# Optimization experiments

Measured on AMD Instinct MI355X. Metric: run time of the kernel, lower is better.

## Reference

```python
import jax, jax.numpy as jnp
import numpy as np

D = 256   # hidden_dim
N = 1024  # total nodes
NP = 384  # paratope nodes
NE = 384  # epitope nodes
NC = 14   # atom channels


def setup_inputs() -> dict:
    key = jax.random.key(0)
    ks = jax.random.split(key, 24)
    s = 1.0 / np.sqrt(D)
    s3 = 1.0 / np.sqrt(3 * D)
    w = lambda k, shape, sc: (jax.random.normal(k, shape, jnp.float32) * sc)
    z = lambda: jnp.zeros((D,), jnp.float32)
    return {
        "H": w(ks[0], (N, D), 1.0),
        "X": w(ks[1], (N, NC, 3), 1.0),
        "paratope_mask": jnp.zeros((N,), bool).at[:NP].set(True),
        "epitope_mask": jnp.zeros((N,), bool).at[NP:NP + NE].set(True),
        "res_w1": w(ks[2], (1, D), 1.0), "res_b1": z(),
        "res_w2": w(ks[3], (D, D), s), "res_b2": z(),
        "atom_w1": w(ks[4], (1, D), 1.0), "atom_b1": z(),
        "atom_w2": w(ks[5], (D, D), s), "atom_b2": z(),
        "sim_weight": jnp.float32(0.5),
        "int_w1": w(ks[6], (3 * D, D), s3), "int_b1": z(),
        "int_w2": w(ks[7], (D, D), s), "int_b2": z(),
        "wl": w(ks[8], (D, D), s),
        "wr": w(ks[9], (D, D), s),
        "wg_w": w(ks[10], (D, D), s), "wg_b": z(),
        "wq_w": w(ks[11], (D, D), s), "wq_b": z(),
        "wk_w": w(ks[12], (D, D), s), "wk_b": z(),
        "wv_w": w(ks[13], (D, D), s), "wv_b": z(),
    }


def _mlp2(x, w1, b1, w2, b2):
    return jax.nn.silu(x @ w1 + b1) @ w2 + b2


def reference(H, X, paratope_mask, epitope_mask,
              res_w1, res_b1, res_w2, res_b2,
              atom_w1, atom_b1, atom_w2, atom_b2,
              sim_weight,
              int_w1, int_b1, int_w2, int_b2,
              wl, wr, wg_w, wg_b, wq_w, wq_b, wk_w, wk_b, wv_w, wv_b):
    p_idx = jnp.nonzero(paratope_mask, size=NP)[0]
    e_idx = jnp.nonzero(epitope_mask, size=NE)[0]
    Hp = H[p_idx]                      # [NP, D]
    He = H[e_idx]                      # [NE, D]
    Xp_ca = X[p_idx, 1]                # [NP, 3] (CA atom)
    Xe_ca = X[e_idx, 1]                # [NE, 3]

    dX = Xp_ca[:, None, :] - Xe_ca[None, :, :]         # [NP, NE, 3]
    S = jnp.sum(dX * dX, axis=-1, keepdims=True)       # [NP, NE, 1]
    # original computes S_residue and S_atom with identical formula
    S_res = _mlp2(S, res_w1, res_b1, res_w2, res_b2)
    S_atom = _mlp2(S, atom_w1, atom_b1, atom_w2, atom_b2)
    wmix = jax.nn.sigmoid(sim_weight)
    S_comb = wmix * S_res + (1.0 - wmix) * S_atom      # [NP, NE, D]

    Hp_e = jnp.broadcast_to(Hp[:, None, :], (NP, NE, D))
    He_e = jnp.broadcast_to(He[None, :, :], (NP, NE, D))
    Z_in = jnp.concatenate([Hp_e, He_e, S_comb], axis=-1)  # [NP, NE, 3D]
    Z = _mlp2(Z_in, int_w1, int_b1, int_w2, int_b2)        # [NP, NE, D]

    I = (Hp @ wl)[:, None, :] * (He @ wr)[None, :, :]      # outer-product interaction
    gate = jax.nn.sigmoid(Z @ wg_w + wg_b)
    f_tri = gate * I

    Q = Z @ wq_w + wq_b
    K = Z @ wk_w + wk_b
    V = Z @ wv_w + wv_b
    scores = jnp.einsum('ped,pfd->pef', Q, K) / (D ** 0.5)  # [NP, NE, NE]
    A = jax.nn.softmax(scores, axis=-1)
    f_att = jnp.einsum('pef,pfd->ped', A, V)

    H_tri = f_tri + f_att                                   # [NP, NE, D]
    return H.at[p_idx].set(H_tri.mean(axis=1))
```

## Files before the change

kernel.cpp:

```cpp
#include <hip/hip_runtime.h>

#define NPAR 384
#define NEPI 384
#define DD   256
#define NTAB 4096
#define SMAX 96.0f
#define SDELTA (SMAX / NTAB)
#define SINVD (NTAB / SMAX)

using bf16x8 = __bf16 __attribute__((ext_vector_type(8)));
using bf16x2 = __bf16 __attribute__((ext_vector_type(2)));
using f32x4  = float __attribute__((ext_vector_type(4)));

#if defined(__has_builtin)
#if __has_builtin(__builtin_amdgcn_cvt_pk_bf16_f32)
#define HAVE_PK_BF16 1
#endif
#endif

__device__ __forceinline__ float sigm(float x) { return 1.0f / (1.0f + __expf(-x)); }
__device__ __forceinline__ float silu(float x) { return x / (1.0f + __expf(-x)); }
__device__ __forceinline__ unsigned short f2bf(float f) {
  unsigned u = __float_as_uint(f);
  u += 0x7fffu + ((u >> 16) & 1u);
  return (unsigned short)(u >> 16);
}
__device__ __forceinline__ float bf2f(unsigned u16) {
  return __uint_as_float(u16 << 16);
}
__device__ __forceinline__ float bf2f_lo(unsigned w) {
  return __uint_as_float(w << 16);
}
__device__ __forceinline__ float bf2f_hi(unsigned w) {
  return __uint_as_float(w & 0xffff0000u);
}
__device__ __forceinline__ uint2 pack4(float a, float b, float c, float d) {
  uint2 r;
#ifdef HAVE_PK_BF16
  bf16x2 lo = __builtin_amdgcn_cvt_pk_bf16_f32(a, b);
  bf16x2 hi = __builtin_amdgcn_cvt_pk_bf16_f32(c, d);
  r.x = __builtin_bit_cast(unsigned, lo);
  r.y = __builtin_bit_cast(unsigned, hi);
#else
  r.x = (unsigned)f2bf(a) | ((unsigned)f2bf(b) << 16);
  r.y = (unsigned)f2bf(c) | ((unsigned)f2bf(d) << 16);
#endif
  return r;
}


__global__ void prep_kernel(
    const float* __restrict__ H, const float* __restrict__ wl,
    const float* __restrict__ wr, const float* __restrict__ int_w1,
    const float* __restrict__ res_w2, const float* __restrict__ atom_w2,
    const float* __restrict__ res_b2, const float* __restrict__ atom_b2,
    const float* __restrict__ int_b1, const float* __restrict__ simw,
    const float* __restrict__ wq_b, const float* __restrict__ wk_w,
    const float* __restrict__ wq_w,
    float* __restrict__ Hpl, float* __restrict__ Her,
    float* __restrict__ P1, float* __restrict__ P2,
    float* __restrict__ MrF, float* __restrict__ MaF,
    float* __restrict__ cvec, float* __restrict__ gv,
    float* __restrict__ WqkF) {
  __shared__ float sbuf[256];
  const int b = blockIdx.x, t = threadIdx.x;
  if (b < 512) {
    const int i = b & 255;
    const bool isMa = b >= 256;
    const float wmix = 1.0f / (1.0f + __expf(-simw[0]));
    const float sc = isMa ? (1.0f - wmix) : wmix;
    const float* W2 = isMa ? atom_w2 : res_w2;
    float acc = 0.f;
#pragma unroll 8
    for (int k = 0; k < 256; ++k)
      acc += W2[i * 256 + k] * int_w1[(512 + k) * 256 + t];
    (isMa ? MaF : MrF)[i * 256 + t] = acc * sc;
  } else if (b == 512) {
    const float wmix = 1.0f / (1.0f + __expf(-simw[0]));
    float acc = int_b1[t];
#pragma unroll 8
    for (int k = 0; k < 256; ++k) {
      float bm = wmix * res_b2[k] + (1.0f - wmix) * atom_b2[k];
      acc += bm * int_w1[(512 + k) * 256 + t];
    }
    cvec[t] = acc;
  } else if (b < 577) {
    const int lane = t & 63, w = t >> 6;
    const int d = (b - 513) * 4 + w;
    float acc = 0.f;
#pragma unroll
    for (int i = 0; i < 4; ++i) {
      const int c = i * 64 + lane;
      acc += wk_w[d * 256 + c] * wq_b[c];
    }
    acc += __shfl_xor(acc, 1);
    acc += __shfl_xor(acc, 2);
    acc += __shfl_xor(acc, 4);
    acc += __shfl_xor(acc, 8);
    acc += __shfl_xor(acc, 16);
    acc += __shfl_xor(acc, 32);
    if (lane == 0) gv[d] = acc;
  } else if (b < 833) {
    const int r = b - 577;
    sbuf[t] = wq_w[r * 256 + t];
    __syncthreads();
    const float* wkrow = wk_w + t * 256;
    float a0 = 0.f, a1 = 0.f, a2 = 0.f, a3 = 0.f;
#pragma unroll 4
    for (int k = 0; k < 256; k += 4) {
      const f32x4 wv4 = *reinterpret_cast<const f32x4*>(&wkrow[k]);
      a0 = fmaf(sbuf[k + 0], wv4[0], a0);
      a1 = fmaf(sbuf[k + 1], wv4[1], a1);
      a2 = fmaf(sbuf[k + 2], wv4[2], a2);
      a3 = fmaf(sbuf[k + 3], wv4[3], a3);
    }
    WqkF[r * 256 + t] = (a0 + a1) + (a2 + a3);
  } else {
    const int idx = b - 833;
    const int seg = idx / 384, r = idx % 384;
    const float* A;
    const float* B;
    float* C;
    switch (seg) {
      case 0:  A = H + r * 256;            B = wl;              C = Hpl + r * 256; break;
      case 1:  A = H + (NPAR + r) * 256;   B = wr;              C = Her + r * 256; break;
      case 2:  A = H + r * 256;            B = int_w1;          C = P1 + r * 256;  break;
      default: A = H + (NPAR + r) * 256;   B = int_w1 + 65536;  C = P2 + r * 256;  break;
    }
    float acc = 0.f;
#pragma unroll 8
    for (int k = 0; k < 256; ++k)
      acc += A[k] * B[k * 256 + t];
    C[t] = acc;
  }
}

__global__ void pack_kernel(const float* __restrict__ MrF, const float* __restrict__ MaF,
                            const float* __restrict__ w2, const float* __restrict__ wg,
                            const float* __restrict__ WqkF, unsigned short* __restrict__ wpack) {
  const int idx = blockIdx.x * 256 + threadIdx.x;
  const int m = idx >> 16;
  const int r = idx & 65535;
  const int chunk = r >> 9;
  const int lane = (r >> 3) & 63;
  const int j = r & 7;
  const int k = (chunk >> 4) * 32 + (lane >> 4) * 8 + j;
  const int n = (chunk & 15) * 16 + (lane & 15);
  const float* src;
  switch (m) {
    case 0: src = MrF; break;
    case 1: src = MaF; break;
    case 2: src = w2; break;
    case 3: src = wg; break;
    default: src = WqkF; break;
  }
  wpack[idx] = f2bf(src[k * 256 + n]);
}


__device__ __forceinline__ void zero_acc4(f32x4 (&acc)[4][4]) {
#pragma unroll
  for (int mt = 0; mt < 4; ++mt)
#pragma unroll
    for (int nt = 0; nt < 4; ++nt)
      acc[mt][nt] = (f32x4){0.f, 0.f, 0.f, 0.f};
}

__device__ __forceinline__ void gemm4(f32x4 (&acc)[4][4],
                                      const unsigned short* __restrict__ wp,
                                      const unsigned short* ub, int lane, int wv) {
  const int l15 = lane & 15, l4 = lane >> 4;
#pragma unroll
  for (int ks = 0; ks < 8; ++ks) {
    bf16x8 a[4];
#pragma unroll
    for (int mt = 0; mt < 4; ++mt)
      a[mt] = *reinterpret_cast<const bf16x8*>(wp + ((ks * 16 + wv * 4 + mt) * 64 + lane) * 8);
#pragma unroll
    for (int nt = 0; nt < 4; ++nt) {
      bf16x8 b = *reinterpret_cast<const bf16x8*>(ub + (nt * 16 + l15) * 264 + ks * 32 + l4 * 8);
#pragma unroll
      for (int mt = 0; mt < 4; ++mt)
        acc[mt][nt] = __builtin_amdgcn_mfma_f32_16x16x32_bf16(a[mt], b, acc[mt][nt], 0, 0, 0);
    }
  }
}

__device__ __forceinline__ void fill_u(unsigned short* ub, const float* Sv,
                                       const float* __restrict__ w1,
                                       const float* __restrict__ b1, int t) {
  const int dg = t & 31, rb = t >> 5;
  const f32x4 w1a = *reinterpret_cast<const f32x4*>(&w1[dg * 8]);
  const f32x4 w1b = *reinterpret_cast<const f32x4*>(&w1[dg * 8 + 4]);
  const f32x4 b1a = *reinterpret_cast<const f32x4*>(&b1[dg * 8]);
  const f32x4 b1b = *reinterpret_cast<const f32x4*>(&b1[dg * 8 + 4]);
#pragma unroll
  for (int i = 0; i < 8; ++i) {
    const int e = rb + i * 8;
    const float s = Sv[e];
    uint2 lo = pack4(silu(fmaf(s, w1a[0], b1a[0])), silu(fmaf(s, w1a[1], b1a[1])),
                     silu(fmaf(s, w1a[2], b1a[2])), silu(fmaf(s, w1a[3], b1a[3])));
    uint2 hi = pack4(silu(fmaf(s, w1b[0], b1b[0])), silu(fmaf(s, w1b[1], b1b[1])),
                     silu(fmaf(s, w1b[2], b1b[2])), silu(fmaf(s, w1b[3], b1b[3])));
    uint4 pk = {lo.x, lo.y, hi.x, hi.y};
    *reinterpret_cast<uint4*>(&ub[e * 264 + dg * 8]) = pk;
  }
}


__global__ __launch_bounds__(256, 3) void tab_kernel(
    const float* __restrict__ res_w1, const float* __restrict__ res_b1,
    const float* __restrict__ atom_w1, const float* __restrict__ atom_b1,
    const unsigned short* __restrict__ wpack, unsigned short* __restrict__ tab) {
  __shared__ __align__(16) unsigned short ubuf[64 * 264];
  __shared__ float Sv[64];
  const int t = threadIdx.x, lane = t & 63, wv = t >> 6;
  const int l15 = lane & 15, l4 = lane >> 4;
  const int n0 = blockIdx.x * 64;
  if (t < 64) Sv[t] = (n0 + t) * SDELTA;
  __syncthreads();
  f32x4 acc[4][4];
  zero_acc4(acc);
  fill_u(ubuf, Sv, res_w1, res_b1, t);
  __syncthreads();
  gemm4(acc, wpack + 0 * 65536, ubuf, lane, wv);
  __syncthreads();
  fill_u(ubuf, Sv, atom_w1, atom_b1, t);
  __syncthreads();
  gemm4(acc, wpack + 1 * 65536, ubuf, lane, wv);
#pragma unroll
  for (int mt = 0; mt < 4; ++mt) {
    const int d = wv * 64 + mt * 16 + l4 * 4;
#pragma unroll
    for (int nt = 0; nt < 4; ++nt) {
      const int n = n0 + nt * 16 + l15;
      *reinterpret_cast<uint2*>(&tab[n * 256 + d]) =
          pack4(acc[mt][nt][0], acc[mt][nt][1], acc[mt][nt][2], acc[mt][nt][3]);
    }
  }
}


__global__ __launch_bounds__(256, 4) void pair_kernel(
    const float* __restrict__ Xg, const unsigned short* __restrict__ tab,
    const float* __restrict__ int_b2, const float* __restrict__ wg_b,
    const unsigned short* __restrict__ wpack, const float* __restrict__ cvec,
    const float* __restrict__ P1, const float* __restrict__ P2,
    const float* __restrict__ Hpl, const float* __restrict__ Her,
    float* __restrict__ ftri, unsigned short* __restrict__ Zsw) {
  __shared__ __align__(16) unsigned short ubuf[64 * 264];
  __shared__ float Sv[64];
  __shared__ float pc[DD];
  const int t = threadIdx.x, lane = t & 63, wv = t >> 6;
  const int l15 = lane & 15, l4 = lane >> 4;
  const int p = blockIdx.x / 6, cc = blockIdx.x % 6, e0 = cc * 64;
  const int d0 = wv * 64;

  if (t < 64) {
    const int e = e0 + t;
    float dx = Xg[p * 42 + 3] - Xg[(NPAR + e) * 42 + 3];
    float dy = Xg[p * 42 + 4] - Xg[(NPAR + e) * 42 + 4];
    float dz = Xg[p * 42 + 5] - Xg[(NPAR + e) * 42 + 5];
    Sv[t] = dx * dx + dy * dy + dz * dz;
  }
  pc[t] = P1[p * DD + t] + cvec[t];
  __syncthreads();

  {
    const int dg = t & 31, rb = t >> 5;
    const f32x4 pca = *reinterpret_cast<const f32x4*>(&pc[dg * 8]);
    const f32x4 pcb = *reinterpret_cast<const f32x4*>(&pc[dg * 8 + 4]);
#pragma unroll
    for (int i = 0; i < 8; ++i) {
      const int e = rb + i * 8;
      float sv = Sv[e] * SINVD;
      int idx = (int)sv;
      idx = idx > (NTAB - 2) ? (NTAB - 2) : idx;
      const float fr = sv - (float)idx;
      const uint4 t0 = *reinterpret_cast<const uint4*>(&tab[idx * 256 + dg * 8]);
      const uint4 t1 = *reinterpret_cast<const uint4*>(&tab[(idx + 1) * 256 + dg * 8]);
      const f32x4 p2a = *reinterpret_cast<const f32x4*>(&P2[(e0 + e) * DD + dg * 8]);
      const f32x4 p2b = *reinterpret_cast<const f32x4*>(&P2[(e0 + e) * DD + dg * 8 + 4]);
      float z0 = bf2f_lo(t0.x), z1 = bf2f_hi(t0.x), z2 = bf2f_lo(t0.y), z3 = bf2f_hi(t0.y);
      float z4 = bf2f_lo(t0.z), z5 = bf2f_hi(t0.z), z6 = bf2f_lo(t0.w), z7 = bf2f_hi(t0.w);
      z0 = fmaf(fr, bf2f_lo(t1.x) - z0, z0) + pca[0] + p2a[0];
      z1 = fmaf(fr, bf2f_hi(t1.x) - z1, z1) + pca[1] + p2a[1];
      z2 = fmaf(fr, bf2f_lo(t1.y) - z2, z2) + pca[2] + p2a[2];
      z3 = fmaf(fr, bf2f_hi(t1.y) - z3, z3) + pca[3] + p2a[3];
      z4 = fmaf(fr, bf2f_lo(t1.z) - z4, z4) + pcb[0] + p2b[0];
      z5 = fmaf(fr, bf2f_hi(t1.z) - z5, z5) + pcb[1] + p2b[1];
      z6 = fmaf(fr, bf2f_lo(t1.w) - z6, z6) + pcb[2] + p2b[2];
      z7 = fmaf(fr, bf2f_hi(t1.w) - z7, z7) + pcb[3] + p2b[3];
      uint2 lo = pack4(silu(z0), silu(z1), silu(z2), silu(z3));
      uint2 hi = pack4(silu(z4), silu(z5), silu(z6), silu(z7));
      uint4 pk = {lo.x, lo.y, hi.x, hi.y};
      *reinterpret_cast<uint4*>(&ubuf[e * 264 + dg * 8]) = pk;
    }
  }
  __syncthreads();

  f32x4 acc[4][4];
  zero_acc4(acc);
  gemm4(acc, wpack + 2 * 65536, ubuf, lane, wv);
  __syncthreads();
#pragma unroll
  for (int mt = 0; mt < 4; ++mt) {
    const int d = d0 + mt * 16 + l4 * 4;
    const f32x4 bb = *reinterpret_cast<const f32x4*>(&int_b2[d]);
#pragma unroll
    for (int nt = 0; nt < 4; ++nt) {
      const int e = nt * 16 + l15;
      *reinterpret_cast<uint2*>(&ubuf[e * 264 + d]) =
          pack4(acc[mt][nt][0] + bb[0], acc[mt][nt][1] + bb[1],
                acc[mt][nt][2] + bb[2], acc[mt][nt][3] + bb[3]);
    }
  }
  __syncthreads();

  {
    unsigned short* Zd = Zsw + (size_t)p * 98304 + (size_t)(cc * 4 + wv) * 4096 + lane * 8;
#pragma unroll
    for (int ks = 0; ks < 8; ++ks) {
      *reinterpret_cast<uint4*>(Zd + ks * 512) =
          *reinterpret_cast<const uint4*>(&ubuf[(wv * 16 + l15) * 264 + ks * 32 + l4 * 8]);
    }
  }

  zero_acc4(acc);
  gemm4(acc, wpack + 3 * 65536, ubuf, lane, wv);
#pragma unroll
  for (int mt = 0; mt < 4; ++mt) {
    const int d = d0 + mt * 16 + l4 * 4;
    const f32x4 bb = *reinterpret_cast<const f32x4*>(&wg_b[d]);
    const f32x4 hl = *reinterpret_cast<const f32x4*>(&Hpl[p * DD + d]);
    f32x4 fs = (f32x4){0.f, 0.f, 0.f, 0.f};
#pragma unroll
    for (int nt = 0; nt < 4; ++nt) {
      const int e = e0 + nt * 16 + l15;
      const f32x4 hr = *reinterpret_cast<const f32x4*>(&Her[e * DD + d]);
#pragma unroll
      for (int r = 0; r < 4; ++r)
        fs[r] += sigm(acc[mt][nt][r] + bb[r]) * hr[r];
    }
#pragma unroll
    for (int r = 0; r < 4; ++r) {
      float v = fs[r] * hl[r];
      v += __shfl_xor(v, 1);
      v += __shfl_xor(v, 2);
      v += __shfl_xor(v, 4);
      v += __shfl_xor(v, 8);
      if (l15 == 0) atomicAdd(&ftri[p * DD + d + r], v);
    }
  }
}


__global__ __launch_bounds__(256, 3) void attn_kernel(
    const unsigned short* __restrict__ Zsw, const float* __restrict__ gv,
    const unsigned short* __restrict__ wpack, float* __restrict__ cbufg) {
  __shared__ __align__(16) unsigned short Tc[64 * 264];
  __shared__ float red[256];
  __shared__ float red2[256];
  const int t = threadIdx.x, lane = t & 63, wv = t >> 6;
  const int l15 = lane & 15, l4 = lane >> 4;
  const int xcd = blockIdx.x & 7, inner = blockIdx.x >> 3;
  const int p = (inner / 6) * 8 + xcd, c = inner % 6;
  const unsigned short* Zsp = Zsw + (size_t)p * 98304;
  const unsigned short* wqk = wpack + 4 * 65536;

  {
    f32x4 ta[4][4];
    zero_acc4(ta);
    const unsigned short* Tb = Zsp + (size_t)(c * 4) * 4096 + lane * 8;
    bf16x8 bcur[4], bnxt[4];
#pragma unroll
    for (int nt = 0; nt < 4; ++nt)
      bcur[nt] = *reinterpret_cast<const bf16x8*>(Tb + nt * 4096);
#pragma unroll
    for (int ks = 0; ks < 8; ++ks) {
      if (ks < 7) {
#pragma unroll
        for (int nt = 0; nt < 4; ++nt)
          bnxt[nt] = *reinterpret_cast<const bf16x8*>(Tb + nt * 4096 + (ks + 1) * 512);
      }
      bf16x8 a[4];
#pragma unroll
      for (int mt = 0; mt < 4; ++mt)
        a[mt] = *reinterpret_cast<const bf16x8*>(wqk + ((ks * 16 + wv * 4 + mt) * 64 + lane) * 8);
#pragma unroll
      for (int nt = 0; nt < 4; ++nt)
#pragma unroll
        for (int mt = 0; mt < 4; ++mt)
          ta[mt][nt] = __builtin_amdgcn_mfma_f32_16x16x32_bf16(a[mt], bcur[nt], ta[mt][nt], 0, 0, 0);
      if (ks < 7) {
#pragma unroll
        for (int nt = 0; nt < 4; ++nt) bcur[nt] = bnxt[nt];
      }
    }
#pragma unroll
    for (int mt = 0; mt < 4; ++mt) {
      const int d = wv * 64 + mt * 16 + l4 * 4;
      const f32x4 gq = *reinterpret_cast<const f32x4*>(&gv[d]);
#pragma unroll
      for (int nt = 0; nt < 4; ++nt) {
        const int e = nt * 16 + l15;
        *reinterpret_cast<uint2*>(&Tc[e * 264 + d]) =
            pack4((ta[mt][nt][0] + gq[0]) * 0.0625f, (ta[mt][nt][1] + gq[1]) * 0.0625f,
                  (ta[mt][nt][2] + gq[2]) * 0.0625f, (ta[mt][nt][3] + gq[3]) * 0.0625f);
      }
    }
  }
  __syncthreads();

  f32x4 sc[4][6];
#pragma unroll
  for (int mt = 0; mt < 4; ++mt)
#pragma unroll
    for (int s = 0; s < 6; ++s) sc[mt][s] = (f32x4){0.f, 0.f, 0.f, 0.f};

  {
    const unsigned short* Sb = Zsp + (size_t)wv * 4096 + lane * 8;
    bf16x8 bcur[6], bnxt[6];
#pragma unroll
    for (int s = 0; s < 6; ++s)
      bcur[s] = *reinterpret_cast<const bf16x8*>(Sb + s * 16384);
#pragma unroll
    for (int ks = 0; ks < 8; ++ks) {
      if (ks < 7) {
#pragma unroll
        for (int s = 0; s < 6; ++s)
          bnxt[s] = *reinterpret_cast<const bf16x8*>(Sb + s * 16384 + (ks + 1) * 512);
      }
      bf16x8 a[4];
#pragma unroll
      for (int mt = 0; mt < 4; ++mt)
        a[mt] = *reinterpret_cast<const bf16x8*>(&Tc[(mt * 16 + l15) * 264 + ks * 32 + l4 * 8]);
#pragma unroll
      for (int s = 0; s < 6; ++s)
#pragma unroll
        for (int mt = 0; mt < 4; ++mt)
          sc[mt][s] = __builtin_amdgcn_mfma_f32_16x16x32_bf16(a[mt], bcur[s], sc[mt][s], 0, 0, 0);
      if (ks < 7) {
#pragma unroll
        for (int s = 0; s < 6; ++s) bcur[s] = bnxt[s];
      }
    }
  }

  float rmax[4][4];
#pragma unroll
  for (int mt = 0; mt < 4; ++mt) {
#pragma unroll
    for (int r = 0; r < 4; ++r) {
      float m = -1e30f;
#pragma unroll
      for (int s = 0; s < 6; ++s) m = fmaxf(m, sc[mt][s][r]);
      m = fmaxf(m, __shfl_xor(m, 1));
      m = fmaxf(m, __shfl_xor(m, 2));
      m = fmaxf(m, __shfl_xor(m, 4));
      m = fmaxf(m, __shfl_xor(m, 8));
      rmax[mt][r] = m;
    }
  }
  if (l15 == 0) {
#pragma unroll
    for (int mt = 0; mt < 4; ++mt)
#pragma unroll
      for (int r = 0; r < 4; ++r)
        red[wv * 64 + mt * 16 + l4 * 4 + r] = rmax[mt][r];
  }
  __syncthreads();
#pragma unroll
  for (int mt = 0; mt < 4; ++mt) {
#pragma unroll
    for (int r = 0; r < 4; ++r) {
      const int row = mt * 16 + l4 * 4 + r;
      rmax[mt][r] = fmaxf(fmaxf(red[row], red[64 + row]), fmaxf(red[128 + row], red[192 + row]));
    }
  }

  float rsum[4][4];
#pragma unroll
  for (int mt = 0; mt < 4; ++mt) {
#pragma unroll
    for (int r = 0; r < 4; ++r) {
      float sSum = 0.f;
#pragma unroll
      for (int s = 0; s < 6; ++s) {
        float e = __expf(sc[mt][s][r] - rmax[mt][r]);
        sc[mt][s][r] = e;
        sSum += e;
      }
      sSum += __shfl_xor(sSum, 1);
      sSum += __shfl_xor(sSum, 2);
      sSum += __shfl_xor(sSum, 4);
      sSum += __shfl_xor(sSum, 8);
      rsum[mt][r] = sSum;
    }
  }
  if (l15 == 0) {
#pragma unroll
    for (int mt = 0; mt < 4; ++mt)
#pragma unroll
      for (int r = 0; r < 4; ++r)
        red2[wv * 64 + mt * 16 + l4 * 4 + r] = rsum[mt][r];
  }
  __syncthreads();
  float rinv[4][4];
#pragma unroll
  for (int mt = 0; mt < 4; ++mt) {
#pragma unroll
    for (int r = 0; r < 4; ++r) {
      const int row = mt * 16 + l4 * 4 + r;
      rinv[mt][r] = 1.0f / (red2[row] + red2[64 + row] + red2[128 + row] + red2[192 + row]);
    }
  }

#pragma unroll
  for (int s = 0; s < 6; ++s) {
    float v = 0.f;
#pragma unroll
    for (int mt = 0; mt < 4; ++mt)
#pragma unroll
      for (int r = 0; r < 4; ++r)
        v += sc[mt][s][r] * rinv[mt][r];
    v += __shfl_xor(v, 16);
    v += __shfl_xor(v, 32);
    if (lane < 16)
      atomicAdd(&cbufg[p * NEPI + s * 64 + wv * 16 + lane], v);
  }
}


__global__ __launch_bounds__(256) void outa_kernel(
    const unsigned short* __restrict__ Zsw, const float* __restrict__ cbufg,
    float* __restrict__ ubufg) {
  __shared__ float cb[128];
  __shared__ float part[16][257];
  const int p = blockIdx.x / 3, th = blockIdx.x % 3, g0 = th * 8;
  const int t = threadIdx.x;
  const int lane = t & 63, wv = t >> 6;
  const int l15 = lane & 15, l4 = lane >> 4;
  if (t < 128) cb[t] = cbufg[p * NEPI + g0 * 16 + t];
  __syncthreads();
  const unsigned short* Zsp = Zsw + (size_t)p * 98304;
  float a16[16];
#pragma unroll
  for (int j = 0; j < 16; ++j) a16[j] = 0.f;
#pragma unroll
  for (int gr = 0; gr < 8; ++gr) {
    const int grp = g0 + gr;
    const float w = cb[gr * 16 + l15];
    const uint4 z0 = *reinterpret_cast<const uint4*>(Zsp + grp * 4096 + wv * 512 + lane * 8);
    const uint4 z1 = *reinterpret_cast<const uint4*>(Zsp + grp * 4096 + (wv + 4) * 512 + lane * 8);
    a16[0] = fmaf(w, bf2f(z0.x & 0xffffu), a16[0]);
    a16[1] = fmaf(w, bf2f(z0.x >> 16), a16[1]);
    a16[2] = fmaf(w, bf2f(z0.y & 0xffffu), a16[2]);
    a16[3] = fmaf(w, bf2f(z0.y >> 16), a16[3]);
    a16[4] = fmaf(w, bf2f(z0.z & 0xffffu), a16[4]);
    a16[5] = fmaf(w, bf2f(z0.z >> 16), a16[5]);
    a16[6] = fmaf(w, bf2f(z0.w & 0xffffu), a16[6]);
    a16[7] = fmaf(w, bf2f(z0.w >> 16), a16[7]);
    a16[8]  = fmaf(w, bf2f(z1.x & 0xffffu), a16[8]);
    a16[9]  = fmaf(w, bf2f(z1.x >> 16), a16[9]);
    a16[10] = fmaf(w, bf2f(z1.y & 0xffffu), a16[10]);
    a16[11] = fmaf(w, bf2f(z1.y >> 16), a16[11]);
    a16[12] = fmaf(w, bf2f(z1.z & 0xffffu), a16[12]);
    a16[13] = fmaf(w, bf2f(z1.z >> 16), a16[13]);
    a16[14] = fmaf(w, bf2f(z1.w & 0xffffu), a16[14]);
    a16[15] = fmaf(w, bf2f(z1.w >> 16), a16[15]);
  }
#pragma unroll
  for (int j = 0; j < 8; ++j) part[l15][wv * 32 + l4 * 8 + j] = a16[j];
#pragma unroll
  for (int j = 0; j < 8; ++j) part[l15][128 + wv * 32 + l4 * 8 + j] = a16[8 + j];
  __syncthreads();
  float uu = 0.f;
#pragma unroll
  for (int g = 0; g < 16; ++g) uu += part[g][t];
  atomicAdd(&ubufg[p * DD + t], uu);
}


__global__ __launch_bounds__(256) void out2_kernel(
    const float* __restrict__ ubufg, const float* __restrict__ ftri,
    const float* __restrict__ wvw, const float* __restrict__ wvb,
    float* __restrict__ out) {
  __shared__ float u[DD];
  const int p = blockIdx.x, t = threadIdx.x;
  u[t] = ubufg[p * DD + t];
  __syncthreads();
  float acc = ftri[p * DD + t] + 384.0f * wvb[t];
#pragma unroll 8
  for (int d = 0; d < DD; ++d)
    acc = fmaf(u[d], wvw[d * DD + t], acc);
  out[p * DD + t] = acc * (1.0f / 384.0f);
}


extern "C" void kernel_launch(void* const* d_in, const int* in_sizes, int n_in,
                              void* d_out, int out_size, void* d_ws, size_t ws_size,
                              hipStream_t stream) {
  (void)in_sizes; (void)n_in; (void)out_size; (void)ws_size;
  const float* H = (const float*)d_in[0];
  const float* X = (const float*)d_in[1];
  const float* res_w1 = (const float*)d_in[4];
  const float* res_b1 = (const float*)d_in[5];
  const float* res_w2 = (const float*)d_in[6];
  const float* res_b2 = (const float*)d_in[7];
  const float* atom_w1 = (const float*)d_in[8];
  const float* atom_b1 = (const float*)d_in[9];
  const float* atom_w2 = (const float*)d_in[10];
  const float* atom_b2 = (const float*)d_in[11];
  const float* simw = (const float*)d_in[12];
  const float* int_w1 = (const float*)d_in[13];
  const float* int_b1 = (const float*)d_in[14];
  const float* int_w2 = (const float*)d_in[15];
  const float* int_b2 = (const float*)d_in[16];
  const float* wl = (const float*)d_in[17];
  const float* wr = (const float*)d_in[18];
  const float* wg_w = (const float*)d_in[19];
  const float* wg_b = (const float*)d_in[20];
  const float* wq_w = (const float*)d_in[21];
  const float* wq_b = (const float*)d_in[22];
  const float* wk_w = (const float*)d_in[23];
  const float* wv_w = (const float*)d_in[25];
  const float* wv_b = (const float*)d_in[26];

  char* ws = (char*)d_ws;
  unsigned short* wpack = (unsigned short*)(ws + 0);
  float* MrF   = (float*)(ws + 655360);
  float* MaF   = (float*)(ws + 917504);
  float* WqkF  = (float*)(ws + 1179648);
  float* cvec  = (float*)(ws + 1441792);
  float* gv    = (float*)(ws + 1442816);
  float* P1    = (float*)(ws + 1443840);
  float* P2    = (float*)(ws + 1837056);
  float* Hpl   = (float*)(ws + 2230272);
  float* Her   = (float*)(ws + 2623488);
  float* ftri  = (float*)(ws + 3016704);
  float* cbufg = (float*)(ws + 3409920);
  float* ubufg = (float*)(ws + 3999744);
  unsigned short* Zsw = (unsigned short*)(ws + 4392960);
  unsigned short* tab = (unsigned short*)(ws + 79890432);

  hipMemsetAsync(ftri, 0, 393216 + 589824 + 393216, stream);
  prep_kernel<<<2369, 256, 0, stream>>>(H, wl, wr, int_w1, res_w2, atom_w2,
                                        res_b2, atom_b2, int_b1, simw, wq_b, wk_w, wq_w,
                                        Hpl, Her, P1, P2, MrF, MaF, cvec, gv, WqkF);
  pack_kernel<<<1280, 256, 0, stream>>>(MrF, MaF, int_w2, wg_w, WqkF, wpack);
  tab_kernel<<<NTAB / 64, 256, 0, stream>>>(res_w1, res_b1, atom_w1, atom_b1, wpack, tab);
  pair_kernel<<<2304, 256, 0, stream>>>(X, tab, int_b2, wg_b, wpack, cvec,
                                        P1, P2, Hpl, Her, ftri, Zsw);
  attn_kernel<<<2304, 256, 0, stream>>>(Zsw, gv, wpack, cbufg);
  outa_kernel<<<1152, 256, 0, stream>>>(Zsw, cbufg, ubufg);
  out2_kernel<<<384, 256, 0, stream>>>(ubufg, ftri, wv_w, wv_b, (float*)d_out);
  hipMemcpyAsync((float*)d_out + NPAR * DD, H + NPAR * DD,
                 (1024 - NPAR) * DD * sizeof(float), hipMemcpyDeviceToDevice, stream);
}
```

Measured before the change: 340.8 us.

## Halve attention query tile per block and register-block prep matvecs

The attention kernel now processes 32 query rows per block instead of 64, doubling the grid to 4608 blocks. It shrinks register and LDS use so launch bounds can ask for 4 blocks per SIMD, and it splits the K-tile loads into two halves to interleave MFMAs with prefetch. Separately, the prep kernel computes 2 or 4 output rows per block, staging the input rows in shared memory so each weight column load is reused across rows. This cuts prep's grid size and global weight traffic. The cost is that each attention block now reloads all of K for only half as many queries, doubling that global/L2 read traffic.

Measured after the change: 335.4 us. Within noise of the previous version (-1.6%).

```diff
diff --git a/kernel.cpp b/kernel.cpp
--- a/kernel.cpp
+++ b/kernel.cpp
@@ -62,20 +62,28 @@
     float* __restrict__ MrF, float* __restrict__ MaF,
     float* __restrict__ cvec, float* __restrict__ gv,
     float* __restrict__ WqkF) {
-  __shared__ float sbuf[256];
+  __shared__ float sbuf[1024];
   const int b = blockIdx.x, t = threadIdx.x;
-  if (b < 512) {
-    const int i = b & 255;
-    const bool isMa = b >= 256;
+  if (b < 256) {
+    const bool isMa = b >= 128;
+    const int i0 = (b & 127) * 2;
     const float wmix = 1.0f / (1.0f + __expf(-simw[0]));
     const float sc = isMa ? (1.0f - wmix) : wmix;
     const float* W2 = isMa ? atom_w2 : res_w2;
-    float acc = 0.f;
+    sbuf[t] = W2[i0 * 256 + t];
+    sbuf[256 + t] = W2[(i0 + 1) * 256 + t];
+    __syncthreads();
+    float a0 = 0.f, a1 = 0.f;
 #pragma unroll 8
-    for (int k = 0; k < 256; ++k)
-      acc += W2[i * 256 + k] * int_w1[(512 + k) * 256 + t];
-    (isMa ? MaF : MrF)[i * 256 + t] = acc * sc;
-  } else if (b == 512) {
+    for (int k = 0; k < 256; ++k) {
+      const float w = int_w1[(512 + k) * 256 + t];
+      a0 = fmaf(sbuf[k], w, a0);
+      a1 = fmaf(sbuf[256 + k], w, a1);
+    }
+    float* dst = isMa ? MaF : MrF;
+    dst[i0 * 256 + t] = a0 * sc;
+    dst[(i0 + 1) * 256 + t] = a1 * sc;
+  } else if (b == 256) {
     const float wmix = 1.0f / (1.0f + __expf(-simw[0]));
     float acc = int_b1[t];
 #pragma unroll 8
@@ -84,9 +92,9 @@
       acc += bm * int_w1[(512 + k) * 256 + t];
     }
     cvec[t] = acc;
-  } else if (b < 577) {
+  } else if (b < 321) {
     const int lane = t & 63, w = t >> 6;
-    const int d = (b - 513) * 4 + w;
+    const int d = (b - 257) * 4 + w;
     float acc = 0.f;
 #pragma unroll
     for (int i = 0; i < 4; ++i) {
@@ -100,8 +108,8 @@
     acc += __shfl_xor(acc, 16);
     acc += __shfl_xor(acc, 32);
     if (lane == 0) gv[d] = acc;
-  } else if (b < 833) {
-    const int r = b - 577;
+  } else if (b < 577) {
+    const int r = b - 321;
     sbuf[t] = wq_w[r * 256 + t];
     __syncthreads();
     const float* wkrow = wk_w + t * 256;
@@ -116,22 +124,33 @@
     }
     WqkF[r * 256 + t] = (a0 + a1) + (a2 + a3);
   } else {
-    const int idx = b - 833;
-    const int seg = idx / 384, r = idx % 384;
+    const int idx = b - 577;
+    const int seg = idx / 96, r0 = (idx % 96) * 4;
     const float* A;
     const float* B;
     float* C;
     switch (seg) {
-      case 0:  A = H + r * 256;            B = wl;              C = Hpl + r * 256; break;
-      case 1:  A = H + (NPAR + r) * 256;   B = wr;              C = Her + r * 256; break;
-      case 2:  A = H + r * 256;            B = int_w1;          C = P1 + r * 256;  break;
-      default: A = H + (NPAR + r) * 256;   B = int_w1 + 65536;  C = P2 + r * 256;  break;
-    }
-    float acc = 0.f;
+      case 0:  A = H + r0 * 256;            B = wl;              C = Hpl + r0 * 256; break;
+      case 1:  A = H + (NPAR + r0) * 256;   B = wr;              C = Her + r0 * 256; break;
+      case 2:  A = H + r0 * 256;            B = int_w1;          C = P1 + r0 * 256;  break;
+      default: A = H + (NPAR + r0) * 256;   B = int_w1 + 65536;  C = P2 + r0 * 256;  break;
+    }
+#pragma unroll
+    for (int j = 0; j < 4; ++j) sbuf[j * 256 + t] = A[j * 256 + t];
+    __syncthreads();
+    float a0 = 0.f, a1 = 0.f, a2 = 0.f, a3 = 0.f;
 #pragma unroll 8
-    for (int k = 0; k < 256; ++k)
-      acc += A[k] * B[k * 256 + t];
-    C[t] = acc;
+    for (int k = 0; k < 256; ++k) {
+      const float bv = B[k * 256 + t];
+      a0 = fmaf(sbuf[k], bv, a0);
+      a1 = fmaf(sbuf[256 + k], bv, a1);
+      a2 = fmaf(sbuf[512 + k], bv, a2);
+      a3 = fmaf(sbuf[768 + k], bv, a3);
+    }
+    C[t] = a0;
+    C[256 + t] = a1;
+    C[512 + t] = a2;
+    C[768 + t] = a3;
   }
 }
 
@@ -355,32 +374,35 @@
 }
 
 
-__global__ __launch_bounds__(256, 3) void attn_kernel(
+__global__ __launch_bounds__(256, 4) void attn_kernel(
     const unsigned short* __restrict__ Zsw, const float* __restrict__ gv,
     const unsigned short* __restrict__ wpack, float* __restrict__ cbufg) {
-  __shared__ __align__(16) unsigned short Tc[64 * 264];
-  __shared__ float red[256];
-  __shared__ float red2[256];
+  __shared__ __align__(16) unsigned short Tc[32 * 264];
+  __shared__ float red[128];
+  __shared__ float red2[128];
   const int t = threadIdx.x, lane = t & 63, wv = t >> 6;
   const int l15 = lane & 15, l4 = lane >> 4;
   const int xcd = blockIdx.x & 7, inner = blockIdx.x >> 3;
-  const int p = (inner / 6) * 8 + xcd, c = inner % 6;
+  const int p = (inner / 12) * 8 + xcd, c = inner % 12;
   const unsigned short* Zsp = Zsw + (size_t)p * 98304;
   const unsigned short* wqk = wpack + 4 * 65536;
 
   {
-    f32x4 ta[4][4];
-    zero_acc4(ta);
-    const unsigned short* Tb = Zsp + (size_t)(c * 4) * 4096 + lane * 8;
-    bf16x8 bcur[4], bnxt[4];
-#pragma unroll
-    for (int nt = 0; nt < 4; ++nt)
+    f32x4 ta[4][2];
+#pragma unroll
+    for (int mt = 0; mt < 4; ++mt)
+#pragma unroll
+      for (int nt = 0; nt < 2; ++nt) ta[mt][nt] = (f32x4){0.f, 0.f, 0.f, 0.f};
+    const unsigned short* Tb = Zsp + (size_t)(c * 2) * 4096 + lane * 8;
+    bf16x8 bcur[2], bnxt[2];
+#pragma unroll
+    for (int nt = 0; nt < 2; ++nt)
       bcur[nt] = *reinterpret_cast<const bf16x8*>(Tb + nt * 4096);
 #pragma unroll
     for (int ks = 0; ks < 8; ++ks) {
       if (ks < 7) {
 #pragma unroll
-        for (int nt = 0; nt < 4; ++nt)
+        for (int nt = 0; nt < 2; ++nt)
           bnxt[nt] = *reinterpret_cast<const bf16x8*>(Tb + nt * 4096 + (ks + 1) * 512);
       }
       bf16x8 a[4];
@@ -388,13 +410,13 @@
       for (int mt = 0; mt < 4; ++mt)
         a[mt] = *reinterpret_cast<const bf16x8*>(wqk + ((ks * 16 + wv * 4 + mt) * 64 + lane) * 8);
 #pragma unroll
-      for (int nt = 0; nt < 4; ++nt)
+      for (int nt = 0; nt < 2; ++nt)
 #pragma unroll
         for (int mt = 0; mt < 4; ++mt)
           ta[mt][nt] = __builtin_amdgcn_mfma_f32_16x16x32_bf16(a[mt], bcur[nt], ta[mt][nt], 0, 0, 0);
       if (ks < 7) {
 #pragma unroll
-        for (int nt = 0; nt < 4; ++nt) bcur[nt] = bnxt[nt];
+        for (int nt = 0; nt < 2; ++nt) bcur[nt] = bnxt[nt];
       }
     }
 #pragma unroll
@@ -402,7 +424,7 @@
       const int d = wv * 64 + mt * 16 + l4 * 4;
       const f32x4 gq = *reinterpret_cast<const f32x4*>(&gv[d]);
 #pragma unroll
-      for (int nt = 0; nt < 4; ++nt) {
+      for (int nt = 0; nt < 2; ++nt) {
         const int e = nt * 16 + l15;
         *reinterpret_cast<uint2*>(&Tc[e * 264 + d]) =
             pack4((ta[mt][nt][0] + gq[0]) * 0.0625f, (ta[mt][nt][1] + gq[1]) * 0.0625f,
@@ -412,44 +434,48 @@
   }
   __syncthreads();
 
-  f32x4 sc[4][6];
-#pragma unroll
-  for (int mt = 0; mt < 4; ++mt)
+  f32x4 sc[2][6];
+#pragma unroll
+  for (int mt = 0; mt < 2; ++mt)
 #pragma unroll
     for (int s = 0; s < 6; ++s) sc[mt][s] = (f32x4){0.f, 0.f, 0.f, 0.f};
 
   {
     const unsigned short* Sb = Zsp + (size_t)wv * 4096 + lane * 8;
-    bf16x8 bcur[6], bnxt[6];
-#pragma unroll
-    for (int s = 0; s < 6; ++s)
-      bcur[s] = *reinterpret_cast<const bf16x8*>(Sb + s * 16384);
+    bf16x8 b0[3], b1[3];
+#pragma unroll
+    for (int j = 0; j < 3; ++j)
+      b0[j] = *reinterpret_cast<const bf16x8*>(Sb + j * 16384);
 #pragma unroll
     for (int ks = 0; ks < 8; ++ks) {
+#pragma unroll
+      for (int j = 0; j < 3; ++j)
+        b1[j] = *reinterpret_cast<const bf16x8*>(Sb + (3 + j) * 16384 + ks * 512);
+      bf16x8 a[2];
+#pragma unroll
+      for (int mt = 0; mt < 2; ++mt)
+        a[mt] = *reinterpret_cast<const bf16x8*>(&Tc[(mt * 16 + l15) * 264 + ks * 32 + l4 * 8]);
+#pragma unroll
+      for (int j = 0; j < 3; ++j)
+#pragma unroll
+        for (int mt = 0; mt < 2; ++mt)
+          sc[mt][j] = __builtin_amdgcn_mfma_f32_16x16x32_bf16(a[mt], b0[j], sc[mt][j], 0, 0, 0);
       if (ks < 7) {
 #pragma unroll
-        for (int s = 0; s < 6; ++s)
-          bnxt[s] = *reinterpret_cast<const bf16x8*>(Sb + s * 16384 + (ks + 1) * 512);
+        for (int j = 0; j < 3; ++j)
+          b0[j] = *reinterpret_cast<const bf16x8*>(Sb + j * 16384 + (ks + 1) * 512);
       }
-      bf16x8 a[4];
-#pragma unroll
-      for (int mt = 0; mt < 4; ++mt)
-        a[mt] = *reinterpret_cast<const bf16x8*>(&Tc[(mt * 16 + l15) * 264 + ks * 32 + l4 * 8]);
-#pragma unroll
-      for (int s = 0; s < 6; ++s)
-#pragma unroll
-        for (int mt = 0; mt < 4; ++mt)
-          sc[mt][s] = __builtin_amdgcn_mfma_f32_16x16x32_bf16(a[mt], bcur[s], sc[mt][s], 0, 0, 0);
-      if (ks < 7) {
-#pragma unroll
-        for (int s = 0; s < 6; ++s) bcur[s] = bnxt[s];
-      }
-    }
-  }
-
-  float rmax[4][4];
-#pragma unroll
-  for (int mt = 0; mt < 4; ++mt) {
+#pragma unroll
+      for (int j = 0; j < 3; ++j)
+#pragma unroll
+        for (int mt = 0; mt < 2; ++mt)
+          sc[mt][3 + j] = __builtin_amdgcn_mfma_f32_16x16x32_bf16(a[mt], b1[j], sc[mt][3 + j], 0, 0, 0);
+    }
+  }
+
+  float rmax[2][4];
+#pragma unroll
+  for (int mt = 0; mt < 2; ++mt) {
 #pragma unroll
     for (int r = 0; r < 4; ++r) {
       float m = -1e30f;
@@ -464,24 +490,24 @@
   }
   if (l15 == 0) {
 #pragma unroll
-    for (int mt = 0; mt < 4; ++mt)
+    for (int mt = 0; mt < 2; ++mt)
 #pragma unroll
       for (int r = 0; r < 4; ++r)
-        red[wv * 64 + mt * 16 + l4 * 4 + r] = rmax[mt][r];
-  }
-  __syncthreads();
-#pragma unroll
-  for (int mt = 0; mt < 4; ++mt) {
+        red[wv * 32 + mt * 16 + l4 * 4 + r] = rmax[mt][r];
+  }
+  __syncthreads();
+#pragma unroll
+  for (int mt = 0; mt < 2; ++mt) {
 #pragma unroll
     for (int r = 0; r < 4; ++r) {
       const int row = mt * 16 + l4 * 4 + r;
-      rmax[mt][r] = fmaxf(fmaxf(red[row], red[64 + row]), fmaxf(red[128 + row], red[192 + row]));
-    }
-  }
-
-  float rsum[4][4];
-#pragma unroll
-  for (int mt = 0; mt < 4; ++mt) {
+      rmax[mt][r] = fmaxf(fmaxf(red[row], red[32 + row]), fmaxf(red[64 + row], red[96 + row]));
+    }
+  }
+
+  float rsum[2][4];
+#pragma unroll
+  for (int mt = 0; mt < 2; ++mt) {
 #pragma unroll
     for (int r = 0; r < 4; ++r) {
       float sSum = 0.f;
@@ -500,19 +526,19 @@
   }
   if (l15 == 0) {
 #pragma unroll
-    for (int mt = 0; mt < 4; ++mt)
+    for (int mt = 0; mt < 2; ++mt)
 #pragma unroll
       for (int r = 0; r < 4; ++r)
-        red2[wv * 64 + mt * 16 + l4 * 4 + r] = rsum[mt][r];
-  }
-  __syncthreads();
-  float rinv[4][4];
-#pragma unroll
-  for (int mt = 0; mt < 4; ++mt) {
+        red2[wv * 32 + mt * 16 + l4 * 4 + r] = rsum[mt][r];
+  }
+  __syncthreads();
+  float rinv[2][4];
+#pragma unroll
+  for (int mt = 0; mt < 2; ++mt) {
 #pragma unroll
     for (int r = 0; r < 4; ++r) {
       const int row = mt * 16 + l4 * 4 + r;
-      rinv[mt][r] = 1.0f / (red2[row] + red2[64 + row] + red2[128 + row] + red2[192 + row]);
+      rinv[mt][r] = 1.0f / (red2[row] + red2[32 + row] + red2[64 + row] + red2[96 + row]);
     }
   }
 
@@ -520,14 +546,14 @@
   for (int s = 0; s < 6; ++s) {
     float v = 0.f;
 #pragma unroll
-    for (int mt = 0; mt < 4; ++mt)
+    for (int mt = 0; mt < 2; ++mt)
 #pragma unroll
       for (int r = 0; r < 4; ++r)
         v += sc[mt][s][r] * rinv[mt][r];
     v += __shfl_xor(v, 16);
     v += __shfl_xor(v, 32);
     if (lane < 16)
-      atomicAdd(&cbufg[p * NEPI + s * 64 + wv * 16 + lane], v);
+      atomicAdd(&cbufg[p * NEPI + (s * 4 + wv) * 16 + lane], v);
   }
 }
 
@@ -645,14 +671,14 @@
   unsigned short* tab = (unsigned short*)(ws + 79890432);
 
   hipMemsetAsync(ftri, 0, 393216 + 589824 + 393216, stream);
-  prep_kernel<<<2369, 256, 0, stream>>>(H, wl, wr, int_w1, res_w2, atom_w2,
-                                        res_b2, atom_b2, int_b1, simw, wq_b, wk_w, wq_w,
-                                        Hpl, Her, P1, P2, MrF, MaF, cvec, gv, WqkF);
+  prep_kernel<<<961, 256, 0, stream>>>(H, wl, wr, int_w1, res_w2, atom_w2,
+                                       res_b2, atom_b2, int_b1, simw, wq_b, wk_w, wq_w,
+                                       Hpl, Her, P1, P2, MrF, MaF, cvec, gv, WqkF);
   pack_kernel<<<1280, 256, 0, stream>>>(MrF, MaF, int_w2, wg_w, WqkF, wpack);
   tab_kernel<<<NTAB / 64, 256, 0, stream>>>(res_w1, res_b1, atom_w1, atom_b1, wpack, tab);
   pair_kernel<<<2304, 256, 0, stream>>>(X, tab, int_b2, wg_b, wpack, cvec,
                                         P1, P2, Hpl, Her, ftri, Zsw);
-  attn_kernel<<<2304, 256, 0, stream>>>(Zsw, gv, wpack, cbufg);
+  attn_kernel<<<4608, 256, 0, stream>>>(Zsw, gv, wpack, cbufg);
   outa_kernel<<<1152, 256, 0, stream>>>(Zsw, cbufg, ubufg);
   out2_kernel<<<384, 256, 0, stream>>>(ubufg, ftri, wv_w, wv_b, (float*)d_out);
   hipMemcpyAsync((float*)d_out + NPAR * DD, H + NPAR * DD,
```
